# Kernel tuning notes

Measured on AMD Instinct MI355X. Metric: run time of the kernel, lower is better.

The kernel has to match this reference:

```python
import jax, jax.numpy as jnp
from jax import lax
import numpy as np

C = 256
K = 80          # num_classes
NL = 4          # num_levels
B = 16
HWS = [80, 40, 20, 10]


def _conv3x3(x, w, b):
    # x: (B,C,H,W), w: (O,I,3,3)
    y = lax.conv_general_dilated(x, w, (1, 1), [(1, 1), (1, 1)],
                                 dimension_numbers=("NCHW", "OIHW", "NCHW"))
    return y + b[None, :, None, None]


def setup_inputs() -> dict:
    key = jax.random.key(0)
    ks = jax.random.split(key, 20)
    d = {}
    for i, hw in enumerate(HWS):
        d[f"feat{i}"] = jax.random.normal(ks[i], (B, C, hw, hw), dtype=jnp.float32)
    s3 = 1.0 / np.sqrt(C * 9)
    sc = 1.0 / np.sqrt(C)
    sh = 1.0 / np.sqrt(C // 4)
    d["conv_w"] = jax.random.normal(ks[4], (C, C, 3, 3), jnp.float32) * s3
    d["conv_b"] = jnp.zeros((C,), jnp.float32)
    d["clsw1"] = jax.random.normal(ks[5], (C // 4, C), jnp.float32) * sc
    d["clsb1"] = jnp.zeros((C // 4,), jnp.float32)
    d["clsw2"] = jax.random.normal(ks[6], (C * K, C // 4), jnp.float32) * sh
    d["clsb2"] = jnp.zeros((C * K,), jnp.float32)
    d["regw1"] = jax.random.normal(ks[7], (C // 4, C), jnp.float32) * sc
    d["regb1"] = jnp.zeros((C // 4,), jnp.float32)
    d["regw2"] = jax.random.normal(ks[8], (C * 4, C // 4), jnp.float32) * sh
    d["regb2"] = jnp.zeros((C * 4,), jnp.float32)
    d["lvl_w"] = jax.random.normal(ks[9], (NL, C), jnp.float32) * sc
    d["lvl_b"] = jnp.zeros((NL,), jnp.float32)
    d["clsf_w"] = jax.random.normal(ks[10], (K, C), jnp.float32) * sc
    d["clsf_b"] = jnp.zeros((K,), jnp.float32)
    d["regf_w"] = jax.random.normal(ks[11], (4, C), jnp.float32) * sc
    d["regf_b"] = jnp.zeros((4,), jnp.float32)
    return d


def _level(feat, i, conv_w, conv_b, clsw1, clsb1, clsw2, clsb2,
           regw1, regb1, regw2, regb2, lvl_w, lvl_b,
           clsf_w, clsf_b, regf_w, regf_b):
    s = jax.nn.relu(_conv3x3(feat, conv_w, conv_b))          # (B,C,H,W)
    p = s.mean(axis=(2, 3))                                  # (B,C) global avg pool
    # dynamic classification weights: (B,C,K)
    hc = jax.nn.relu(p @ clsw1.T + clsb1)
    cw = (hc @ clsw2.T + clsb2).reshape(p.shape[0], C, K)
    hr = jax.nn.relu(p @ regw1.T + regb1)
    rw = (hr @ regw2.T + regb2).reshape(p.shape[0], C, 4)
    # fused broadcast-mul-sum over channels -> batched contraction
    cls_feat = jnp.einsum("bchw,bck->bkhw", s, cw)
    reg_feat = jnp.einsum("bchw,bck->bkhw", s, rw)
    cls_out = jnp.einsum("bchw,kc->bkhw", s, clsf_w) + clsf_b[None, :, None, None] + cls_feat
    reg_out = jnp.einsum("bchw,kc->bkhw", s, regf_w) + regf_b[None, :, None, None] + reg_feat
    att = jax.nn.softmax(p @ lvl_w.T + lvl_b, axis=1)[:, i]  # (B,)
    att = att[:, None, None, None]
    return cls_out * att, reg_out * att


def reference(feat0, feat1, feat2, feat3, conv_w, conv_b, clsw1, clsb1,
              clsw2, clsb2, regw1, regb1, regw2, regb2, lvl_w, lvl_b,
              clsf_w, clsf_b, regf_w, regf_b):
    feats = [feat0, feat1, feat2, feat3]
    outs = [_level(f, i, conv_w, conv_b, clsw1, clsb1, clsw2, clsb2,
                   regw1, regb1, regw2, regb2, lvl_w, lvl_b,
                   clsf_w, clsf_b, regf_w, regf_b)
            for i, f in enumerate(feats)]
    cls_logits = tuple(o[0] for o in outs)
    bbox_preds = tuple(o[1] for o in outs)
    return cls_logits + bbox_preds
```

## Files before the change

### kernel.cpp

```cpp
#include <hip/hip_runtime.h>
#include <math.h>

typedef __attribute__((ext_vector_type(8))) short bf16x8;
typedef __attribute__((ext_vector_type(4))) float f32x4;
typedef unsigned int uint32;

#define OFFB_WT3   0LL
#define OFFB_PT    1179648LL
#define OFFB_WEFFM 1179648LL
#define OFFB_ST    75857920LL
#define OFFB_PP    145489920LL
#define OFFB_P     150405120LL
#define OFFB_BEFF  150470656LL
#define OFFB_HB    150492160LL


__device__ inline unsigned short f2bf(float f) {
    uint32 u = __float_as_uint(f);
    uint32 r = (u + 0x7fffu + ((u >> 16) & 1u)) >> 16;
    return (unsigned short)r;
}

__device__ void prep_w_worker(int co, int ci, const float* __restrict__ w,
                              unsigned short* __restrict__ WT3) {
    int half = ci >> 7, cc = ci & 127, c8 = cc >> 3, j = cc & 7;
    const float* src = w + ((size_t)co * 256 + ci) * 9;
#pragma unroll
    for (int tap = 0; tap < 9; ++tap) {
        int q = (half * 9 + tap) * 16 + c8;
        WT3[((size_t)q * 256 + co) * 8 + j] = f2bf(src[tap]);
    }
}

template<int H, int W>
__device__ void pad_worker(int bid, int t, const float* __restrict__ feat,
                           unsigned short* __restrict__ PT, unsigned short* lds) {
    constexpr int WP = W + 2;
    int y = bid % (H + 2), b = bid / (H + 2);
    unsigned short* dst = PT + ((size_t)(b * (H + 2) + y)) * WP * 256;
    if (y == 0 || y == H + 1) {
        for (int e = t; e < WP * 256; e += 256) dst[e] = 0;
        return;
    }
    const float* src = feat + ((size_t)b * 256) * (H * W) + (size_t)(y - 1) * W;
    for (int e = t; e < 256 * W; e += 256) {
        int ci = e / W, x = e - ci * W;
        lds[ci * (W + 1) + x] = f2bf(src[(size_t)ci * H * W + x]);
    }
    __syncthreads();
    for (int e = t; e < WP * 256; e += 256) {
        int x = e >> 8, ci = e & 255;
        dst[e] = (x == 0 || x == W + 1) ? (unsigned short)0 : lds[ci * (W + 1) + x - 1];
    }
}

__global__ __launch_bounds__(256) void prep_pad_kernel(
    const float* __restrict__ conv_w,
    const float* __restrict__ feat0, const float* __restrict__ feat1,
    const float* __restrict__ feat2, const float* __restrict__ feat3,
    unsigned short* __restrict__ WT3, unsigned short* __restrict__ PT)
{
    __shared__ unsigned short lds[256 * 81];
    int bid = blockIdx.x;
    int t = threadIdx.x;
    if (bid < 256)        { prep_w_worker(bid, t, conv_w, WT3); }
    else if (bid < 1568)  { pad_worker<80,80>(bid - 256,  t, feat0, PT,              lds); }
    else if (bid < 2240)  { pad_worker<40,40>(bid - 1568, t, feat1, PT + 27541504LL, lds); }
    else if (bid < 2592)  { pad_worker<20,20>(bid - 2240, t, feat2, PT + 34766848LL, lds); }
    else                  { pad_worker<10,10>(bid - 2592, t, feat3, PT + 36749312LL, lds); }
}

template<int H, int W, int NF, int WL>
__device__ void conv_worker(int bid, int tid,
    const unsigned short* __restrict__ PT,
    const unsigned short* __restrict__ WT3,
    const float* __restrict__ cbias,
    unsigned short* __restrict__ ST,
    float* __restrict__ pp,
    unsigned short* smem)
{
    constexpr int WP = W + 2;
    constexpr int NPX = H * W;
    constexpr int SLOTS = 3 * WL * 16;

    int h = bid % H, b = bid / H;
    int lane = tid & 63, wv = tid >> 6;
    int g = lane >> 4, l15 = lane & 15;
    int co0 = wv * 32;

    f32x4 acc[2][NF];
#pragma unroll
    for (int m = 0; m < 2; ++m)
#pragma unroll
        for (int n = 0; n < NF; ++n) acc[m][n] = (f32x4)0.0f;

    const unsigned short* ptrow = PT + (size_t)(b * (H + 2) + h) * WP * 256;

    for (int half = 0; half < 2; ++half) {
        if (half) __syncthreads();
        for (int s = tid; s < SLOTS; s += 512) {
            int r = s / (WL * 16);
            int rem = s - r * (WL * 16);
            int x = rem >> 4, cb = rem & 15;
            int xc = x < WP ? x : WP - 1;
            bf16x8 v = *(const bf16x8*)(ptrow + ((size_t)r * WP + xc) * 256 + half * 128 + cb * 8);
            *(bf16x8*)(smem + (((r * WL + x) * 16) + (cb ^ (x & 15))) * 8) = v;
        }
        __syncthreads();

#pragma unroll
        for (int ky = 0; ky < 3; ++ky) {
#pragma unroll
            for (int kx = 0; kx < 3; ++kx) {
#pragma unroll
                for (int cs = 0; cs < 4; ++cs) {
                    int q = (half * 9 + ky * 3 + kx) * 16 + cs * 4 + g;
                    const unsigned short* ap = WT3 + ((size_t)q * 256 + co0 + l15) * 8;
                    bf16x8 a0 = *(const bf16x8*)(ap);
                    bf16x8 a1 = *(const bf16x8*)(ap + 128);
#pragma unroll
                    for (int nf = 0; nf < NF; ++nf) {
                        int xi = nf * 16 + l15 + kx;
                        bf16x8 bv = *(const bf16x8*)(smem +
                            (((ky * WL + xi) * 16) + ((cs * 4 + g) ^ (xi & 15))) * 8);
                        acc[0][nf] = __builtin_amdgcn_mfma_f32_16x16x32_bf16(a0, bv, acc[0][nf], 0, 0, 0);
                        acc[1][nf] = __builtin_amdgcn_mfma_f32_16x16x32_bf16(a1, bv, acc[1][nf], 0, 0, 0);
                    }
                }
            }
        }
    }

    float cb4[2][4];
#pragma unroll
    for (int m = 0; m < 2; ++m)
#pragma unroll
        for (int j = 0; j < 4; ++j)
            cb4[m][j] = cbias[co0 + m * 16 + g * 4 + j];

    float rs[2][4];
#pragma unroll
    for (int m = 0; m < 2; ++m)
#pragma unroll
        for (int j = 0; j < 4; ++j) rs[m][j] = 0.f;

    __syncthreads();
    unsigned short* lds_t = smem;

#pragma unroll
    for (int m = 0; m < 2; ++m) {
#pragma unroll
        for (int nf = 0; nf < NF; ++nf) {
            int px = nf * 16 + l15;
            bool ok = (px < W);
            short4 o;
#pragma unroll
            for (int j = 0; j < 4; ++j) {
                float v = acc[m][nf][j] + cb4[m][j];
                v = v > 0.f ? v : 0.f;
                if (ok) rs[m][j] += v;
                ((short*)&o)[j] = (short)f2bf(v);
            }
            if (ok) *(short4*)(lds_t + px * 260 + co0 + m * 16 + g * 4) = o;
        }
    }
#pragma unroll
    for (int m = 0; m < 2; ++m)
#pragma unroll
        for (int j = 0; j < 4; ++j) {
            float r = rs[m][j];
            r += __shfl_xor(r, 1);
            r += __shfl_xor(r, 2);
            r += __shfl_xor(r, 4);
            r += __shfl_xor(r, 8);
            if (l15 == 0)
                pp[((size_t)b * H + h) * 256 + co0 + m * 16 + g * 4 + j] = r;
        }
    __syncthreads();
    unsigned short* strow = ST + ((size_t)b * NPX + (size_t)h * W) * 256;
    for (int e = tid; e < W * 64; e += 512) {
        int px = e >> 6, c4 = e & 63;
        short4 v = *(const short4*)(lds_t + px * 260 + c4 * 4);
        *(short4*)(strow + (size_t)px * 256 + c4 * 4) = v;
    }
}

__global__ __launch_bounds__(512) void conv_all_kernel(
    const unsigned short* __restrict__ PT, const unsigned short* __restrict__ WT3,
    const float* __restrict__ cbias, unsigned short* __restrict__ ST,
    float* __restrict__ pp)
{
    __shared__ unsigned short smem[3 * 84 * 128];
    int bid = blockIdx.x;
    int tid = threadIdx.x;
    if (bid < 1280) {
        conv_worker<80,80,5,84>(bid, tid, PT, WT3, cbias, ST, pp, smem);
    } else if (bid < 1920) {
        conv_worker<40,40,3,52>(bid - 1280, tid, PT + 27541504LL, WT3, cbias,
                                ST + 26214400LL, pp + 327680, smem);
    } else if (bid < 2240) {
        conv_worker<20,20,2,36>(bid - 1920, tid, PT + 34766848LL, WT3, cbias,
                                ST + 32768000LL, pp + 491520, smem);
    } else {
        conv_worker<10,10,1,20>(bid - 2240, tid, PT + 36749312LL, WT3, cbias,
                                ST + 34406400LL, pp + 573440, smem);
    }
}

__global__ __launch_bounds__(256) void pool2_kernel(const float* __restrict__ pp,
                                                    float* __restrict__ p) {
    const int rows_[4] = {80, 40, 20, 10};
    const int base_[4] = {0, 327680, 491520, 573440};
    const float inv_[4] = {1.f / 6400.f, 1.f / 1600.f, 1.f / 400.f, 1.f / 100.f};
    int lvl = blockIdx.x >> 4;
    int b   = blockIdx.x & 15;
    int t   = threadIdx.x;
    int rows = rows_[lvl];
    const float* src = pp + base_[lvl] + ((size_t)b * rows) * 256 + t;
    float s = 0.f;
    for (int r = 0; r < rows; ++r) s += src[r * 256];
    p[(lvl * 16 + b) * 256 + t] = s * inv_[lvl];
}

__global__ __launch_bounds__(256) void head1_kernel(
    const float* __restrict__ p,
    const float* __restrict__ clsw1, const float* __restrict__ clsb1,
    const float* __restrict__ regw1, const float* __restrict__ regb1,
    const float* __restrict__ lvlw,  const float* __restrict__ lvlb,
    const float* __restrict__ clsfb, const float* __restrict__ regfb,
    float* __restrict__ hb, float* __restrict__ beff)
{
    int lvl = blockIdx.x >> 4;
    int b   = blockIdx.x & 15;
    int t   = threadIdx.x;
    __shared__ float pl[256];
    __shared__ float lgl[4];
    __shared__ float attl;

    pl[t] = p[(lvl * 16 + b) * 256 + t];
    __syncthreads();

    float hval = 0.f;
    if (t < 64) {
        float a = clsb1[t];
        const float* wr = clsw1 + t * 256;
        for (int c2 = 0; c2 < 256; ++c2) a = fmaf(pl[c2], wr[c2], a);
        hval = a > 0.f ? a : 0.f;
    } else if (t < 128) {
        int j = t - 64;
        float a = regb1[j];
        const float* wr = regw1 + j * 256;
        for (int c2 = 0; c2 < 256; ++c2) a = fmaf(pl[c2], wr[c2], a);
        hval = a > 0.f ? a : 0.f;
    } else if (t < 132) {
        int j = t - 128;
        float a = lvlb[j];
        const float* wr = lvlw + j * 256;
        for (int c2 = 0; c2 < 256; ++c2) a = fmaf(pl[c2], wr[c2], a);
        lgl[j] = a;
    }
    __syncthreads();
    if (t == 0) {
        float m = fmaxf(fmaxf(lgl[0], lgl[1]), fmaxf(lgl[2], lgl[3]));
        float e0 = expf(lgl[0] - m), e1 = expf(lgl[1] - m);
        float e2 = expf(lgl[2] - m), e3 = expf(lgl[3] - m);
        float se = e0 + e1 + e2 + e3;
        float el = (lvl == 0) ? e0 : (lvl == 1) ? e1 : (lvl == 2) ? e2 : e3;
        attl = el / se;
    }
    __syncthreads();
    float att = attl;

    size_t base = (size_t)(lvl * 16 + b) * 136;
    if (t < 128) hb[base + t] = hval;
    else if (t == 128) hb[base + 128] = att;
    if (t < 84) {
        beff[(lvl * 16 + b) * 84 + t] = att * (t < 80 ? clsfb[t] : regfb[t - 80]);
    }
}

__global__ __launch_bounds__(256) void weff2_kernel(
    const float* __restrict__ hb,
    const float* __restrict__ clsw2, const float* __restrict__ clsb2,
    const float* __restrict__ regw2, const float* __restrict__ regb2,
    const float* __restrict__ clsfw, const float* __restrict__ regfw,
    unsigned short* __restrict__ weffM)
{
    int c = blockIdx.x;
    int t = threadIdx.x;
    __shared__ float wlds[84 * 64];
    __shared__ float hcs[64 * 65];
    __shared__ float hrs[64 * 65];
    __shared__ float atts[64];
    __shared__ float cst[84];

    {
        const float4* csrc = (const float4*)(clsw2 + (size_t)c * 80 * 64);
        float4* wd = (float4*)wlds;
        for (int e = t; e < 80 * 16; e += 256) wd[e] = csrc[e];
        const float4* rsrc = (const float4*)(regw2 + (size_t)c * 4 * 64);
        for (int e = t; e < 4 * 16; e += 256) wd[80 * 16 + e] = rsrc[e];
    }
    for (int e = t; e < 64 * 64; e += 256) {
        int lb = e >> 6, j = e & 63;
        hcs[lb * 65 + j] = hb[(size_t)lb * 136 + j];
        hrs[lb * 65 + j] = hb[(size_t)lb * 136 + 64 + j];
    }
    if (t < 64) atts[t] = hb[(size_t)t * 136 + 128];
    if (t < 84) {
        cst[t] = (t < 80) ? (clsb2[(size_t)c * 80 + t] + clsfw[(size_t)t * 256 + c])
                          : (regb2[(size_t)c * 4 + (t - 80)] + regfw[(size_t)(t - 80) * 256 + c]);
    }
    __syncthreads();

    int lb = t & 63;
    int kg0 = t >> 6;
    const float* hc = hcs + lb * 65;
    const float* hr = hrs + lb * 65;
    float att = atts[lb];
    unsigned short* ob = weffM + (size_t)lb * 24576;

    for (int kg = kg0; kg < 21; kg += 4) {
        const float* h = (kg == 20) ? hr : hc;
        const float* wr = wlds + kg * 4 * 64;
        float a0 = 0.f, a1 = 0.f, a2 = 0.f, a3 = 0.f;
#pragma unroll
        for (int j = 0; j < 64; ++j) {
            float hj = h[j];
            a0 = fmaf(hj, wr[j], a0);
            a1 = fmaf(hj, wr[64 + j], a1);
            a2 = fmaf(hj, wr[128 + j], a2);
            a3 = fmaf(hj, wr[192 + j], a3);
        }
        int k = kg * 4;
        ob[(size_t)(k + 0) * 256 + c] = f2bf(att * (cst[k + 0] + a0));
        ob[(size_t)(k + 1) * 256 + c] = f2bf(att * (cst[k + 1] + a1));
        ob[(size_t)(k + 2) * 256 + c] = f2bf(att * (cst[k + 2] + a2));
        ob[(size_t)(k + 3) * 256 + c] = f2bf(att * (cst[k + 3] + a3));
    }
    for (int e = t; e < 64 * 12; e += 256) {
        int lb2 = e / 12, k2 = 84 + (e - lb2 * 12);
        weffM[(size_t)lb2 * 24576 + (size_t)k2 * 256 + c] = 0;
    }
}

__global__ __launch_bounds__(512) void epilogue_mfma_kernel(
    const unsigned short* __restrict__ ST, const unsigned short* __restrict__ weffM,
    const float* __restrict__ beff, float* __restrict__ out)
{
    int bid = blockIdx.x;
    int lvl, tiles, rem;
    if (bid < 400)      { lvl = 0; tiles = 25; rem = bid; }
    else if (bid < 512) { lvl = 1; tiles = 7;  rem = bid - 400; }
    else if (bid < 544) { lvl = 2; tiles = 2;  rem = bid - 512; }
    else                { lvl = 3; tiles = 1;  rem = bid - 544; }
    const int npx_[4] = {6400, 1600, 400, 100};
    const long long stb_[4] = {0LL, 26214400LL, 32768000LL, 34406400LL};
    const int cb_[4]  = {0, 8192000, 10240000, 10752000};
    const int rb_[4]  = {10880000, 11289600, 11392000, 11417600};
    int npx  = npx_[lvl];
    int tile = rem % tiles;
    int b    = rem / tiles;
    int lb   = lvl * 16 + b;
    int px0  = tile * 256;

    int tid = threadIdx.x;
    int lane = tid & 63, wv = tid >> 6;
    int g = lane >> 4, l15 = lane & 15;

    __shared__ unsigned short walds[96 * 256];
    __shared__ unsigned short slds[256 * 32];

    const unsigned short* wsrc = weffM + (size_t)lb * 24576;
    for (int e = tid; e < 96 * 32; e += 512) {
        int row = e >> 5, ch = e & 31;
        bf16x8 v = *(const bf16x8*)(wsrc + (size_t)row * 256 + ch * 8);
        int chp = (ch & 16) | ((ch & 15) ^ (row & 15));
        *(bf16x8*)(walds + row * 256 + chp * 8) = v;
    }

    f32x4 acc[6][2];
#pragma unroll
    for (int m = 0; m < 6; ++m) { acc[m][0] = (f32x4)0.0f; acc[m][1] = (f32x4)0.0f; }

    const unsigned short* stB = ST + stb_[lvl] + ((size_t)b * npx + px0) * 256;

    for (int kk = 0; kk < 8; ++kk) {
        __syncthreads();
        for (int pr = tid; pr < 1024; pr += 512) {
            int px = pr >> 2, e = pr & 3;
            bf16x8 v = *(const bf16x8*)(stB + (size_t)px * 256 + kk * 32 + e * 8);
            *(bf16x8*)(slds + px * 32 + ((e ^ ((px >> 1) & 3)) * 8)) = v;
        }
        __syncthreads();

        bf16x8 af[6];
#pragma unroll
        for (int m = 0; m < 6; ++m) {
            int row = m * 16 + l15;
            int chA = kk * 4 + g;
            int chp = (chA & 16) | ((chA & 15) ^ (row & 15));
            af[m] = *(const bf16x8*)(walds + row * 256 + chp * 8);
        }
#pragma unroll
        for (int nn = 0; nn < 2; ++nn) {
            int px = wv * 32 + nn * 16 + l15;
            bf16x8 bf = *(const bf16x8*)(slds + px * 32 + ((g ^ ((px >> 1) & 3)) * 8));
#pragma unroll
            for (int m = 0; m < 6; ++m)
                acc[m][nn] = __builtin_amdgcn_mfma_f32_16x16x32_bf16(af[m], bf, acc[m][nn], 0, 0, 0);
        }
    }

    const float* lbeff = beff + (size_t)lb * 84;
#pragma unroll
    for (int m = 0; m < 6; ++m) {
#pragma unroll
        for (int nn = 0; nn < 2; ++nn) {
            int px = px0 + wv * 32 + nn * 16 + l15;
            if (px >= npx) continue;
#pragma unroll
            for (int j = 0; j < 4; ++j) {
                int k = m * 16 + g * 4 + j;
                if (k >= 84) continue;
                float v = acc[m][nn][j] + lbeff[k];
                float* op;
                if (k < 80) op = out + cb_[lvl] + ((size_t)b * 80 + k) * npx + px;
                else        op = out + rb_[lvl] + ((size_t)b * 4 + (k - 80)) * npx + px;
                *op = v;
            }
        }
    }
}

extern "C" void kernel_launch(void* const* d_in, const int* in_sizes, int n_in,
                              void* d_out, int out_size, void* d_ws, size_t ws_size,
                              hipStream_t stream) {
    (void)in_sizes; (void)n_in; (void)out_size; (void)ws_size;
    const float* feat0  = (const float*)d_in[0];
    const float* feat1  = (const float*)d_in[1];
    const float* feat2  = (const float*)d_in[2];
    const float* feat3  = (const float*)d_in[3];
    const float* conv_w = (const float*)d_in[4];
    const float* conv_b = (const float*)d_in[5];
    const float* clsw1  = (const float*)d_in[6];
    const float* clsb1  = (const float*)d_in[7];
    const float* clsw2  = (const float*)d_in[8];
    const float* clsb2  = (const float*)d_in[9];
    const float* regw1  = (const float*)d_in[10];
    const float* regb1  = (const float*)d_in[11];
    const float* regw2  = (const float*)d_in[12];
    const float* regb2  = (const float*)d_in[13];
    const float* lvlw   = (const float*)d_in[14];
    const float* lvlb   = (const float*)d_in[15];
    const float* clsfw  = (const float*)d_in[16];
    const float* clsfb  = (const float*)d_in[17];
    const float* regfw  = (const float*)d_in[18];
    const float* regfb  = (const float*)d_in[19];

    char* ws = (char*)d_ws;
    unsigned short* WT3   = (unsigned short*)(ws + OFFB_WT3);
    unsigned short* PT    = (unsigned short*)(ws + OFFB_PT);
    unsigned short* weffM = (unsigned short*)(ws + OFFB_WEFFM);
    unsigned short* ST    = (unsigned short*)(ws + OFFB_ST);
    float*          pp    = (float*)(ws + OFFB_PP);
    float*          p     = (float*)(ws + OFFB_P);
    float*          beff  = (float*)(ws + OFFB_BEFF);
    float*          hb    = (float*)(ws + OFFB_HB);
    float* out = (float*)d_out;

    hipLaunchKernelGGL(prep_pad_kernel, dim3(2784), dim3(256), 0, stream,
                       conv_w, feat0, feat1, feat2, feat3, WT3, PT);

    hipLaunchKernelGGL(conv_all_kernel, dim3(2400), dim3(512), 0, stream,
                       PT, WT3, conv_b, ST, pp);

    hipLaunchKernelGGL(pool2_kernel, dim3(64), dim3(256), 0, stream, pp, p);
    hipLaunchKernelGGL(head1_kernel, dim3(64), dim3(256), 0, stream, p,
                       clsw1, clsb1, regw1, regb1, lvlw, lvlb, clsfb, regfb, hb, beff);
    hipLaunchKernelGGL(weff2_kernel, dim3(256), dim3(256), 0, stream, hb,
                       clsw2, clsb2, regw2, regb2, clsfw, regfw, weffM);
    hipLaunchKernelGGL(epilogue_mfma_kernel, dim3(560), dim3(512), 0, stream, ST, weffM, beff, out);
}
```

Before: 324.3 us.

## Split level-0 conv rows into half-width tiles and fuse pooling into head kernel

The level-0 conv now splits each 80-pixel row into two 40-pixel tiles. This shrinks the shared-memory staging buffer and raises the block count, which should give better occupancy and load balance. Per-tile partial sums go to pp, and the separate pooling kernel is folded into the head1 kernel, removing one launch and one intermediate buffer. In exchange, level-0 does padded MFMA work (48 computed pixels per 40-pixel tile) and reloads weights for each tile.

New measurement: 407.5 us. 1.26x slower.

```diff
diff --git a/kernel.cpp b/kernel.cpp
--- a/kernel.cpp
+++ b/kernel.cpp
@@ -70,7 +70,7 @@
     else                  { pad_worker<10,10>(bid - 2592, t, feat3, PT + 36749312LL, lds); }
 }
 
-template<int H, int W, int NF, int WL>
+template<int H, int W, int TW, int NF, int WL, int NT>
 __device__ void conv_worker(int bid, int tid,
     const unsigned short* __restrict__ PT,
     const unsigned short* __restrict__ WT3,
@@ -83,7 +83,10 @@
     constexpr int NPX = H * W;
     constexpr int SLOTS = 3 * WL * 16;
 
-    int h = bid % H, b = bid / H;
+    int tile = bid % NT;
+    int h = (bid / NT) % H;
+    int b = bid / (NT * H);
+    int px0 = tile * TW;
     int lane = tid & 63, wv = tid >> 6;
     int g = lane >> 4, l15 = lane & 15;
     int co0 = wv * 32;
@@ -102,7 +105,8 @@
             int r = s / (WL * 16);
             int rem = s - r * (WL * 16);
             int x = rem >> 4, cb = rem & 15;
-            int xc = x < WP ? x : WP - 1;
+            int xc = px0 + x;
+            if (xc >= WP) xc = WP - 1;
             bf16x8 v = *(const bf16x8*)(ptrow + ((size_t)r * WP + xc) * 256 + half * 128 + cb * 8);
             *(bf16x8*)(smem + (((r * WL + x) * 16) + (cb ^ (x & 15))) * 8) = v;
         }
@@ -152,7 +156,7 @@
 #pragma unroll
         for (int nf = 0; nf < NF; ++nf) {
             int px = nf * 16 + l15;
-            bool ok = (px < W);
+            bool ok = (px < TW);
             short4 o;
 #pragma unroll
             for (int j = 0; j < 4; ++j) {
@@ -174,11 +178,11 @@
             r += __shfl_xor(r, 4);
             r += __shfl_xor(r, 8);
             if (l15 == 0)
-                pp[((size_t)b * H + h) * 256 + co0 + m * 16 + g * 4 + j] = r;
-        }
-    __syncthreads();
-    unsigned short* strow = ST + ((size_t)b * NPX + (size_t)h * W) * 256;
-    for (int e = tid; e < W * 64; e += 512) {
+                pp[(((size_t)b * H + h) * NT + tile) * 256 + co0 + m * 16 + g * 4 + j] = r;
+        }
+    __syncthreads();
+    unsigned short* strow = ST + ((size_t)b * NPX + (size_t)h * W + px0) * 256;
+    for (int e = tid; e < TW * 64; e += 512) {
         int px = e >> 6, c4 = e & 63;
         short4 v = *(const short4*)(lds_t + px * 260 + c4 * 4);
         *(short4*)(strow + (size_t)px * 256 + c4 * 4) = v;
@@ -190,46 +194,34 @@
     const float* __restrict__ cbias, unsigned short* __restrict__ ST,
     float* __restrict__ pp)
 {
-    __shared__ unsigned short smem[3 * 84 * 128];
+    __shared__ unsigned short smem[3 * 52 * 128];
     int bid = blockIdx.x;
     int tid = threadIdx.x;
-    if (bid < 1280) {
-        conv_worker<80,80,5,84>(bid, tid, PT, WT3, cbias, ST, pp, smem);
-    } else if (bid < 1920) {
-        conv_worker<40,40,3,52>(bid - 1280, tid, PT + 27541504LL, WT3, cbias,
-                                ST + 26214400LL, pp + 327680, smem);
-    } else if (bid < 2240) {
-        conv_worker<20,20,2,36>(bid - 1920, tid, PT + 34766848LL, WT3, cbias,
-                                ST + 32768000LL, pp + 491520, smem);
+    if (bid < 2560) {
+        conv_worker<80,80,40,3,52,2>(bid, tid, PT, WT3, cbias, ST, pp, smem);
+    } else if (bid < 3200) {
+        conv_worker<40,40,40,3,52,1>(bid - 2560, tid, PT + 27541504LL, WT3, cbias,
+                                     ST + 26214400LL, pp + 655360, smem);
+    } else if (bid < 3520) {
+        conv_worker<20,20,20,2,36,1>(bid - 3200, tid, PT + 34766848LL, WT3, cbias,
+                                     ST + 32768000LL, pp + 819200, smem);
     } else {
-        conv_worker<10,10,1,20>(bid - 2240, tid, PT + 36749312LL, WT3, cbias,
-                                ST + 34406400LL, pp + 573440, smem);
-    }
-}
-
-__global__ __launch_bounds__(256) void pool2_kernel(const float* __restrict__ pp,
-                                                    float* __restrict__ p) {
-    const int rows_[4] = {80, 40, 20, 10};
-    const int base_[4] = {0, 327680, 491520, 573440};
-    const float inv_[4] = {1.f / 6400.f, 1.f / 1600.f, 1.f / 400.f, 1.f / 100.f};
-    int lvl = blockIdx.x >> 4;
-    int b   = blockIdx.x & 15;
-    int t   = threadIdx.x;
-    int rows = rows_[lvl];
-    const float* src = pp + base_[lvl] + ((size_t)b * rows) * 256 + t;
-    float s = 0.f;
-    for (int r = 0; r < rows; ++r) s += src[r * 256];
-    p[(lvl * 16 + b) * 256 + t] = s * inv_[lvl];
-}
-
-__global__ __launch_bounds__(256) void head1_kernel(
-    const float* __restrict__ p,
+        conv_worker<10,10,10,1,20,1>(bid - 3520, tid, PT + 36749312LL, WT3, cbias,
+                                     ST + 34406400LL, pp + 901120, smem);
+    }
+}
+
+__global__ __launch_bounds__(256) void pool_head_kernel(
+    const float* __restrict__ pp,
     const float* __restrict__ clsw1, const float* __restrict__ clsb1,
     const float* __restrict__ regw1, const float* __restrict__ regb1,
     const float* __restrict__ lvlw,  const float* __restrict__ lvlb,
     const float* __restrict__ clsfb, const float* __restrict__ regfb,
     float* __restrict__ hb, float* __restrict__ beff)
 {
+    const int rows_[4] = {160, 40, 20, 10};
+    const int base_[4] = {0, 655360, 819200, 901120};
+    const float inv_[4] = {1.f / 6400.f, 1.f / 1600.f, 1.f / 400.f, 1.f / 100.f};
     int lvl = blockIdx.x >> 4;
     int b   = blockIdx.x & 15;
     int t   = threadIdx.x;
@@ -237,7 +229,13 @@
     __shared__ float lgl[4];
     __shared__ float attl;
 
-    pl[t] = p[(lvl * 16 + b) * 256 + t];
+    {
+        int rows = rows_[lvl];
+        const float* src = pp + base_[lvl] + ((size_t)b * rows) * 256 + t;
+        float s = 0.f;
+        for (int r = 0; r < rows; ++r) s += src[r * 256];
+        pl[t] = s * inv_[lvl];
+    }
     __syncthreads();
 
     float hval = 0.f;
@@ -464,7 +462,6 @@
     unsigned short* weffM = (unsigned short*)(ws + OFFB_WEFFM);
     unsigned short* ST    = (unsigned short*)(ws + OFFB_ST);
     float*          pp    = (float*)(ws + OFFB_PP);
-    float*          p     = (float*)(ws + OFFB_P);
     float*          beff  = (float*)(ws + OFFB_BEFF);
     float*          hb    = (float*)(ws + OFFB_HB);
     float* out = (float*)d_out;
@@ -472,11 +469,10 @@
     hipLaunchKernelGGL(prep_pad_kernel, dim3(2784), dim3(256), 0, stream,
                        conv_w, feat0, feat1, feat2, feat3, WT3, PT);
 
-    hipLaunchKernelGGL(conv_all_kernel, dim3(2400), dim3(512), 0, stream,
+    hipLaunchKernelGGL(conv_all_kernel, dim3(3680), dim3(512), 0, stream,
                        PT, WT3, conv_b, ST, pp);
 
-    hipLaunchKernelGGL(pool2_kernel, dim3(64), dim3(256), 0, stream, pp, p);
-    hipLaunchKernelGGL(head1_kernel, dim3(64), dim3(256), 0, stream, p,
+    hipLaunchKernelGGL(pool_head_kernel, dim3(64), dim3(256), 0, stream, pp,
                        clsw1, clsb1, regw1, regb1, lvlw, lvlb, clsfb, regfb, hb, beff);
     hipLaunchKernelGGL(weff2_kernel, dim3(256), dim3(256), 0, stream, hb,
                        clsw2, clsb2, regw2, regb2, clsfw, regfw, weffM);
```
